# Optimization experiments

Hardware: AMD Instinct MI355X
Metric: run time of the kernel (lower is better)

## Reference

```python
import jax, jax.numpy as jnp
import numpy as np

H = 512      # hidden_size
FF = 4 * H   # expert FFN inner dim
E = 8        # expert_num
K = 2        # top_k
B, S = 4, 4096


def setup_inputs() -> dict:
    key = jax.random.key(0)
    ks = jax.random.split(key, 4)
    s = 0.02
    return {
        "x":  jax.random.normal(ks[0], (B, S, H), dtype=jnp.float32),
        "Wg": jax.random.normal(ks[1], (H, E), dtype=jnp.float32) * s,
        "bg": jnp.zeros((E,), dtype=jnp.float32),
        "W1": jax.random.normal(ks[2], (E, H, FF), dtype=jnp.float32) * s,
        "b1": jnp.zeros((E, FF), dtype=jnp.float32),
        "W2": jax.random.normal(ks[3], (E, FF, H), dtype=jnp.float32) * s,
        "b2": jnp.zeros((E, H), dtype=jnp.float32),
    }


def reference(x, Wg, bg, W1, b1, W2, b2):
    # gate + top-k routing
    logits = x @ Wg + bg                               # [B,S,E]
    w, idx = jax.lax.top_k(logits, K)                  # [B,S,K]
    w = jax.nn.softmax(w, axis=-1)                     # softmax over top-k logits

    # naive dense MoE: every expert runs on every token (matches torch source)
    h = jax.nn.silu(jnp.einsum('bsh,ehf->ebsf', x, W1) + b1[:, None, None, :])  # [E,B,S,FF]
    y = jnp.einsum('ebsf,efh->ebsh', h, W2) + b2[:, None, None, :]              # [E,B,S,H]

    # one-hot mask * top-k weight, combined over slots (same math as torch loop)
    comb = jnp.einsum('bske,bsk->ebs', jax.nn.one_hot(idx, E, dtype=x.dtype), w)  # [E,B,S]
    return jnp.einsum('ebsh,ebs->bsh', y, comb)        # [B,S,H]
```

## Files before the change

kernel.cpp:

```cpp
#include <hip/hip_runtime.h>
#include <hip/hip_bf16.h>
#include <math.h>


#define T_TOK 16384
#define H_DIM 512
#define FF_DIM 2048
#define E_NUM 8
#define NSLOT (T_TOK * 2)
#define NB_ROUTE 128

typedef __attribute__((ext_vector_type(4))) float f32x4;
typedef __attribute__((ext_vector_type(8))) short s16x8;

__device__ __forceinline__ void gload_lds16(const void* g, void* l) {
    __builtin_amdgcn_global_load_lds((const __attribute__((address_space(1))) void*)g,
                                     (__attribute__((address_space(3))) void*)l, 16, 0, 0);
}

__device__ __forceinline__ unsigned short f2bf(float f) {
    union { float f; unsigned int u; } a; a.f = f;
    unsigned int r = a.u + 0x7FFF + ((a.u >> 16) & 1);
    return (unsigned short)(r >> 16);
}


__global__ __launch_bounds__(256) void zero_f32(float* p, int n) {
    int i = (blockIdx.x * 256 + threadIdx.x) * 4;
    if (i < n) { f32x4 z = {0.f, 0.f, 0.f, 0.f}; *(f32x4*)(p + i) = z; }
}

__global__ __launch_bounds__(256) void transpose_bf16(const float* __restrict__ src,
                                                      unsigned short* __restrict__ dst,
                                                      int R, int C) {
    const int e = blockIdx.z;
    const int c0 = blockIdx.x * 32, r0 = blockIdx.y * 32;
    __shared__ float tile[32][33];
    const float* s = src + (size_t)e * R * C;
    unsigned short* d = dst + (size_t)e * R * C;
    const int tid = threadIdx.x;
    for (int idx = tid; idx < 1024; idx += 256) {
        int r = idx >> 5, c = idx & 31;
        tile[r][c] = s[(size_t)(r0 + r) * C + c0 + c];
    }
    __syncthreads();
    for (int idx = tid; idx < 1024; idx += 256) {
        int r = idx >> 5, c = idx & 31;
        d[(size_t)(c0 + r) * R + r0 + c] = f2bf(tile[c][r]);
    }
}

__global__ __launch_bounds__(256) void gather_a(const unsigned short* __restrict__ xb,
                                                const int* __restrict__ slot_token,
                                                unsigned short* __restrict__ Ax) {
    const int gid = blockIdx.x * 256 + threadIdx.x;
    const int s = gid >> 6;
    const int o = (gid & 63) * 8;
    const int t = slot_token[s];
    *(s16x8*)&Ax[(size_t)s * H_DIM + o] = *(const s16x8*)&xb[(size_t)t * H_DIM + o];
}


__global__ __launch_bounds__(256) void gate_topk(const float* __restrict__ x,
                                                 const float* __restrict__ Wg,
                                                 const float* __restrict__ bg,
                                                 int* __restrict__ eidx,
                                                 float* __restrict__ ewt,
                                                 unsigned short* __restrict__ xb) {
    const int t = blockIdx.x * 4 + (threadIdx.x >> 6);
    const int l = threadIdx.x & 63;
    const float* xr = x + (size_t)t * H_DIM;
    unsigned short* xw = xb + (size_t)t * H_DIM;
    double part[E_NUM];
#pragma unroll
    for (int e = 0; e < E_NUM; ++e) part[e] = 0.0;
#pragma unroll
    for (int i = 0; i < 8; ++i) {
        const int h = l + 64 * i;
        const float xv = xr[h];
        xw[h] = f2bf(xv);
        const double xd = (double)xv;
        const float* wr = Wg + (size_t)h * E_NUM;
#pragma unroll
        for (int e = 0; e < E_NUM; ++e) part[e] += xd * (double)wr[e];
    }
    for (int s = 1; s < 64; s <<= 1) {
#pragma unroll
        for (int e = 0; e < E_NUM; ++e) part[e] += __shfl_xor(part[e], s);
    }
    if (l == 0) {
        double lg[E_NUM];
#pragma unroll
        for (int e = 0; e < E_NUM; ++e) lg[e] = part[e] + (double)bg[e];
        int e0 = 0;
        for (int e = 1; e < E_NUM; ++e) if (lg[e] > lg[e0]) e0 = e;
        int e1 = (e0 == 0) ? 1 : 0;
        for (int e = 0; e < E_NUM; ++e) if (e != e0 && lg[e] > lg[e1]) e1 = e;
        double z = exp(lg[e1] - lg[e0]);
        float w0 = (float)(1.0 / (1.0 + z));
        float w1 = (float)(z / (1.0 + z));
        eidx[2 * t] = e0; eidx[2 * t + 1] = e1;
        ewt[2 * t] = w0; ewt[2 * t + 1] = w1;
    }
}


__global__ __launch_bounds__(256) void count_blocks(const int* __restrict__ eidx,
                                                    int* __restrict__ blockcnt) {
    __shared__ int cnt[E_NUM];
    if (threadIdx.x < E_NUM) cnt[threadIdx.x] = 0;
    __syncthreads();
    const int s = blockIdx.x * 256 + threadIdx.x;
    atomicAdd(&cnt[eidx[s]], 1);
    __syncthreads();
    if (threadIdx.x < E_NUM)
        blockcnt[blockIdx.x * E_NUM + threadIdx.x] = cnt[threadIdx.x];
}

__global__ __launch_bounds__(512) void scan_blocks(const int* __restrict__ blockcnt,
                                                   int* __restrict__ bbase,
                                                   int* __restrict__ offsets) {
    __shared__ int tot[E_NUM];
    __shared__ int obase[E_NUM + 1];
    const int e = threadIdx.x >> 6;
    const int l = threadIdx.x & 63;
    const int a = blockcnt[(2 * l) * E_NUM + e];
    const int b = blockcnt[(2 * l + 1) * E_NUM + e];
    const int s = a + b;
    int sc = s;
    for (int d = 1; d < 64; d <<= 1) {
        int o = __shfl_up(sc, d);
        if (l >= d) sc += o;
    }
    const int excl = sc - s;
    if (l == 63) tot[e] = sc;
    __syncthreads();
    if (threadIdx.x == 0) {
        int acc = 0;
        for (int i = 0; i < E_NUM; ++i) { obase[i] = acc; acc += tot[i]; }
        obase[E_NUM] = acc;
        for (int i = 0; i <= E_NUM; ++i) offsets[i] = obase[i];
    }
    __syncthreads();
    const int base = obase[e] + excl;
    bbase[(2 * l) * E_NUM + e] = base;
    bbase[(2 * l + 1) * E_NUM + e] = base + a;
}

__global__ __launch_bounds__(256) void scatter_slots(const int* __restrict__ eidx,
                                                     const float* __restrict__ ewt,
                                                     const int* __restrict__ bbase,
                                                     int* __restrict__ slot_token,
                                                     float* __restrict__ slot_w,
                                                     int* __restrict__ slot_of) {
    __shared__ int cur[E_NUM];
    if (threadIdx.x < E_NUM)
        cur[threadIdx.x] = bbase[blockIdx.x * E_NUM + threadIdx.x];
    __syncthreads();
    const int s = blockIdx.x * 256 + threadIdx.x;
    const int e = eidx[s];
    const int pos = atomicAdd(&cur[e], 1);
    slot_token[pos] = s >> 1;
    slot_w[pos] = ewt[s];
    slot_of[s] = pos;
}


template<int EPI, int GAT, int NT, int KD, int NTOT, int MC, int LDA>
__global__ __launch_bounds__(256, 3) void ggemm(
    const unsigned short* __restrict__ Ag,
    const unsigned short* __restrict__ Bt,
    const float* __restrict__ bias,
    const int* __restrict__ slot_token,
    const float* __restrict__ slot_w,
    const int* __restrict__ offsets,
    unsigned short* __restrict__ Hout,
    float* __restrict__ out) {
    const int e = blockIdx.x;
    const int nt = blockIdx.y % NT;
    const int mc = blockIdx.y / NT;
    const int base = offsets[e];
    const int cnt = offsets[e + 1] - base;
    if (cnt == 0) return;
    const int n0 = nt * 128;

    __shared__ __align__(16) unsigned short Abuf[128 * 64];
    __shared__ __align__(16) unsigned short Bbuf[128 * 64];

    const int tid = threadIdx.x;
    const int w = tid >> 6;
    const int l = tid & 63;
    const int wm = (w & 1) << 6;
    const int wn = (w >> 1) << 6;

    int aoff[4], boff[4];
#pragma unroll
    for (int i = 0; i < 4; ++i) {
        int r = wm + i * 16 + (l & 15);
        aoff[i] = r * 128 + ((((l >> 4) ^ (r & 7))) << 4);
    }
#pragma unroll
    for (int j = 0; j < 4; ++j) {
        int r = wn + j * 16 + (l & 15);
        boff[j] = r * 128 + ((((l >> 4) ^ (r & 7))) << 4);
    }

    const int srow = tid >> 3;
    const int sce = (tid & 7) * 8;
    const unsigned short* Bg = Bt + (size_t)e * NTOT * KD + (size_t)n0 * KD;
    const int nk = KD / 64;

    int bsrc[4];
#pragma unroll
    for (int p = 0; p < 4; ++p) {
        int row = p * 32 + srow;
        bsrc[p] = (row & ~63) | ((row & 15) << 2) | ((row >> 4) & 3);
    }

    for (int m0 = mc * 128; m0 < cnt; m0 += MC * 128) {
        int arow[4];
#pragma unroll
        for (int p = 0; p < 4; ++p) {
            int s = m0 + p * 32 + srow;
            if (s > cnt - 1) s = cnt - 1;
            arow[p] = GAT ? slot_token[base + s] : (base + s);
        }

        f32x4 acc[4][4] = {};
        for (int kt = 0; kt < nk; ++kt) {
            const int k0 = kt * 64;
            __syncthreads();
#pragma unroll
            for (int p = 0; p < 4; ++p) {
                int row = p * 32 + srow;
                int ce = sce ^ ((row & 7) * 8);
                gload_lds16(Ag + (size_t)arow[p] * LDA + k0 + ce, &Abuf[row * 64 + sce]);
                gload_lds16(Bg + (size_t)bsrc[p] * KD + k0 + ce, &Bbuf[row * 64 + sce]);
            }
            __syncthreads();
            const char* Ab = (const char*)&Abuf[0];
            const char* Bb = (const char*)&Bbuf[0];
#pragma unroll
            for (int half = 0; half < 2; ++half) {
                const int kb = half << 6;
                s16x8 af[4], bfv[4];
#pragma unroll
                for (int i = 0; i < 4; ++i) af[i] = *(const s16x8*)(Ab + (aoff[i] ^ kb));
#pragma unroll
                for (int j = 0; j < 4; ++j) bfv[j] = *(const s16x8*)(Bb + (boff[j] ^ kb));
#pragma unroll
                for (int i = 0; i < 4; ++i)
#pragma unroll
                    for (int j = 0; j < 4; ++j)
                        acc[i][j] = __builtin_amdgcn_mfma_f32_16x16x32_bf16(af[i], bfv[j], acc[i][j], 0, 0, 0);
            }
        }

        const int c0 = wn + (l & 15) * 4;
        float b4[4];
#pragma unroll
        for (int j = 0; j < 4; ++j) b4[j] = bias[(size_t)e * NTOT + n0 + c0 + j];

#pragma unroll
        for (int i = 0; i < 4; ++i) {
            const int rb = wm + i * 16 + ((l >> 4) << 2);
#pragma unroll
            for (int r = 0; r < 4; ++r) {
                const int row = m0 + rb + r;
                if (row >= cnt) continue;
                const int slot = base + row;
                if (EPI == 0) {
                    float v0 = acc[i][0][r] + b4[0];
                    float v1 = acc[i][1][r] + b4[1];
                    float v2 = acc[i][2][r] + b4[2];
                    float v3 = acc[i][3][r] + b4[3];
                    v0 = v0 / (1.0f + __expf(-v0));
                    v1 = v1 / (1.0f + __expf(-v1));
                    v2 = v2 / (1.0f + __expf(-v2));
                    v3 = v3 / (1.0f + __expf(-v3));
                    uint2 pk;
                    pk.x = (unsigned int)f2bf(v0) | ((unsigned int)f2bf(v1) << 16);
                    pk.y = (unsigned int)f2bf(v2) | ((unsigned int)f2bf(v3) << 16);
                    *(uint2*)&Hout[(size_t)slot * NTOT + n0 + c0] = pk;
                } else if (EPI == 2) {
                    const float wgt = slot_w[slot];
                    f32x4 v;
#pragma unroll
                    for (int j = 0; j < 4; ++j) v[j] = wgt * (acc[i][j][r] + b4[j]);
                    *(f32x4*)&out[(size_t)slot * NTOT + n0 + c0] = v;
                } else {
                    const int tok = slot_token[slot];
                    const float wgt = slot_w[slot];
                    float* op = out + (size_t)tok * NTOT + n0 + c0;
#pragma unroll
                    for (int j = 0; j < 4; ++j)
                        atomicAdd(op + j, wgt * (acc[i][j][r] + b4[j]));
                }
            }
        }
        __syncthreads();
    }
}

__global__ __launch_bounds__(256) void combine_y(const float* __restrict__ Y,
                                                 const int* __restrict__ slot_of,
                                                 float* __restrict__ out) {
    const int idx = blockIdx.x * 256 + threadIdx.x;
    const int t = idx >> 6;
    const int h = (idx & 63) * 8;
    const int sa = slot_of[2 * t];
    const int sb = slot_of[2 * t + 1];
    const float* pa = Y + (size_t)sa * H_DIM + h;
    const float* pb = Y + (size_t)sb * H_DIM + h;
    f32x4 a0 = *(const f32x4*)pa, a1 = *(const f32x4*)(pa + 4);
    f32x4 b0 = *(const f32x4*)pb, b1 = *(const f32x4*)(pb + 4);
    float* po = out + (size_t)t * H_DIM + h;
    *(f32x4*)po = a0 + b0;
    *(f32x4*)(po + 4) = a1 + b1;
}


extern "C" void kernel_launch(void* const* d_in, const int* in_sizes, int n_in,
                              void* d_out, int out_size, void* d_ws, size_t ws_size,
                              hipStream_t stream) {
    const float* x  = (const float*)d_in[0];
    const float* Wg = (const float*)d_in[1];
    const float* bg = (const float*)d_in[2];
    const float* W1 = (const float*)d_in[3];
    const float* b1 = (const float*)d_in[4];
    const float* W2 = (const float*)d_in[5];
    const float* b2 = (const float*)d_in[6];
    float* out = (float*)d_out;

    char* ws = (char*)d_ws;
    size_t off = 0;
    auto take = [&](size_t b) -> void* {
        void* p = ws + off;
        off = (off + b + 255) & ~(size_t)255;
        return p;
    };
    unsigned short* xb   = (unsigned short*)take((size_t)T_TOK * H_DIM * 2);
    unsigned short* W1t  = (unsigned short*)take((size_t)E_NUM * H_DIM * FF_DIM * 2);
    unsigned short* W2t  = (unsigned short*)take((size_t)E_NUM * H_DIM * FF_DIM * 2);
    int*   eidx       = (int*)take((size_t)T_TOK * 2 * 4);
    float* ewt        = (float*)take((size_t)T_TOK * 2 * 4);
    int*   slot_token = (int*)take((size_t)NSLOT * 4);
    float* slot_w     = (float*)take((size_t)NSLOT * 4);
    int*   slot_of    = (int*)take((size_t)NSLOT * 4);
    int*   blockcnt   = (int*)take((size_t)NB_ROUTE * E_NUM * 4);
    int*   bbase      = (int*)take((size_t)NB_ROUTE * E_NUM * 4);
    int*   offsets    = (int*)take(256);
    unsigned short* Hact = (unsigned short*)take((size_t)NSLOT * FF_DIM * 2);
    float* Yf = (float*)take((size_t)NSLOT * H_DIM * 4);
    const int useY = (ws_size >= off) ? 1 : 0;
    unsigned short* Ax = (unsigned short*)(ws + off);
    const int useAx = (ws_size >= off + (size_t)NSLOT * H_DIM * 2) ? 1 : 0;

    transpose_bf16<<<dim3(FF_DIM / 32, H_DIM / 32, E_NUM), 256, 0, stream>>>(W1, W1t, H_DIM, FF_DIM);
    transpose_bf16<<<dim3(H_DIM / 32, FF_DIM / 32, E_NUM), 256, 0, stream>>>(W2, W2t, FF_DIM, H_DIM);

    gate_topk<<<T_TOK / 4, 256, 0, stream>>>(x, Wg, bg, eidx, ewt, xb);
    count_blocks<<<NB_ROUTE, 256, 0, stream>>>(eidx, blockcnt);
    scan_blocks<<<1, 512, 0, stream>>>(blockcnt, bbase, offsets);
    scatter_slots<<<NB_ROUTE, 256, 0, stream>>>(eidx, ewt, bbase, slot_token, slot_w, slot_of);

    if (useAx) {
        gather_a<<<NSLOT * 64 / 256, 256, 0, stream>>>(xb, slot_token, Ax);
        ggemm<0, 0, 16, 512, 2048, 16, 512><<<dim3(8, 256), 256, 0, stream>>>(
            Ax, W1t, b1, slot_token, slot_w, offsets, Hact, out);
    } else {
        ggemm<0, 1, 16, 512, 2048, 16, 512><<<dim3(8, 256), 256, 0, stream>>>(
            xb, W1t, b1, slot_token, slot_w, offsets, Hact, out);
    }
    if (useY) {
        ggemm<2, 0, 4, 2048, 512, 32, 2048><<<dim3(8, 128), 256, 0, stream>>>(
            Hact, W2t, b2, slot_token, slot_w, offsets, Hact, Yf);
        combine_y<<<T_TOK * 64 / 256, 256, 0, stream>>>(Yf, slot_of, out);
    } else {
        zero_f32<<<(T_TOK * H_DIM / 4 + 255) / 256, 256, 0, stream>>>(out, T_TOK * H_DIM);
        ggemm<1, 0, 4, 2048, 512, 32, 2048><<<dim3(8, 128), 256, 0, stream>>>(
            Hact, W2t, b2, slot_token, slot_w, offsets, Hact, out);
    }
    (void)in_sizes; (void)n_in; (void)out_size;
}
```

Baseline: 318.8 us.

## Enlarge grouped GEMM tiles to 256x256 with double-buffered LDS prefetch

Rewrites the grouped expert GEMM to use 512-thread blocks computing 256x256 tiles, with LDS double buffering. Global-to-LDS loads for the next K tiles are interleaved with MFMA quarters, using explicit vmcnt waits, barriers and setprio. The larger tiles are meant to raise data reuse and hide memory latency behind compute. In exchange, occupancy drops to one block per CU with 128KB of LDS, and the much smaller grid (e.g. 8x32 blocks for the second GEMM) may leave CUs idle given per-expert imbalance.

Result: slower. 421.2 us (+32.1%).

```diff
diff --git a/kernel.cpp b/kernel.cpp
--- a/kernel.cpp
+++ b/kernel.cpp
@@ -166,8 +166,8 @@
 }
 
 
-template<int EPI, int GAT, int NT, int KD, int NTOT, int MC, int LDA>
-__global__ __launch_bounds__(256, 3) void ggemm(
+template<int EPI, int GAT, int NT, int KD, int NTOT, int MCB, int LDA>
+__global__ __launch_bounds__(512, 1) void ggemm(
     const unsigned short* __restrict__ Ag,
     const unsigned short* __restrict__ Bt,
     const float* __restrict__ bias,
@@ -182,20 +182,20 @@
     const int base = offsets[e];
     const int cnt = offsets[e + 1] - base;
     if (cnt == 0) return;
-    const int n0 = nt * 128;
-
-    __shared__ __align__(16) unsigned short Abuf[128 * 64];
-    __shared__ __align__(16) unsigned short Bbuf[128 * 64];
+    const int n0 = nt * 256;
+
+    __shared__ __align__(16) unsigned short Abuf[2][256 * 64];
+    __shared__ __align__(16) unsigned short Bbuf[2][256 * 64];
 
     const int tid = threadIdx.x;
     const int w = tid >> 6;
     const int l = tid & 63;
-    const int wm = (w & 1) << 6;
-    const int wn = (w >> 1) << 6;
-
-    int aoff[4], boff[4];
-#pragma unroll
-    for (int i = 0; i < 4; ++i) {
+    const int wm = (w >> 2) << 7;
+    const int wn = (w & 3) << 6;
+
+    int aoff[8], boff[4];
+#pragma unroll
+    for (int i = 0; i < 8; ++i) {
         int r = wm + i * 16 + (l & 15);
         aoff[i] = r * 128 + ((((l >> 4) ^ (r & 7))) << 4);
     }
@@ -207,54 +207,93 @@
 
     const int srow = tid >> 3;
     const int sce = (tid & 7) * 8;
+    int srow4[4], sceX[4];
+#pragma unroll
+    for (int p = 0; p < 4; ++p) {
+        srow4[p] = p * 64 + srow;
+        sceX[p] = sce ^ ((srow4[p] & 7) * 8);
+    }
     const unsigned short* Bg = Bt + (size_t)e * NTOT * KD + (size_t)n0 * KD;
     const int nk = KD / 64;
 
     int bsrc[4];
 #pragma unroll
     for (int p = 0; p < 4; ++p) {
-        int row = p * 32 + srow;
+        int row = srow4[p];
         bsrc[p] = (row & ~63) | ((row & 15) << 2) | ((row >> 4) & 3);
     }
 
-    for (int m0 = mc * 128; m0 < cnt; m0 += MC * 128) {
+    for (int m0 = mc * 256; m0 < cnt; m0 += MCB * 256) {
         int arow[4];
 #pragma unroll
         for (int p = 0; p < 4; ++p) {
-            int s = m0 + p * 32 + srow;
+            int s = m0 + srow4[p];
             if (s > cnt - 1) s = cnt - 1;
             arow[p] = GAT ? slot_token[base + s] : (base + s);
         }
 
-        f32x4 acc[4][4] = {};
+#define STAGE_A(tile, p) gload_lds16(Ag + (size_t)arow[p] * LDA + (tile) * 64 + sceX[p], \
+                                     &Abuf[(tile) & 1][srow4[p] * 64 + sce])
+#define STAGE_B(tile, p) gload_lds16(Bg + (size_t)bsrc[p] * KD + (tile) * 64 + sceX[p], \
+                                     &Bbuf[(tile) & 1][srow4[p] * 64 + sce])
+
+#pragma unroll
+        for (int p = 0; p < 4; ++p) { STAGE_A(0, p); STAGE_B(0, p); }
+#pragma unroll
+        for (int p = 0; p < 4; ++p) STAGE_B(1, p);
+        STAGE_A(1, 0); STAGE_A(1, 2);
+        asm volatile("s_waitcnt vmcnt(6)" ::: "memory");
+        __builtin_amdgcn_s_barrier();
+
+        f32x4 acc[8][4] = {};
         for (int kt = 0; kt < nk; ++kt) {
-            const int k0 = kt * 64;
-            __syncthreads();
-#pragma unroll
-            for (int p = 0; p < 4; ++p) {
-                int row = p * 32 + srow;
-                int ce = sce ^ ((row & 7) * 8);
-                gload_lds16(Ag + (size_t)arow[p] * LDA + k0 + ce, &Abuf[row * 64 + sce]);
-                gload_lds16(Bg + (size_t)bsrc[p] * KD + k0 + ce, &Bbuf[row * 64 + sce]);
-            }
-            __syncthreads();
-            const char* Ab = (const char*)&Abuf[0];
-            const char* Bb = (const char*)&Bbuf[0];
-#pragma unroll
-            for (int half = 0; half < 2; ++half) {
-                const int kb = half << 6;
-                s16x8 af[4], bfv[4];
-#pragma unroll
-                for (int i = 0; i < 4; ++i) af[i] = *(const s16x8*)(Ab + (aoff[i] ^ kb));
-#pragma unroll
-                for (int j = 0; j < 4; ++j) bfv[j] = *(const s16x8*)(Bb + (boff[j] ^ kb));
-#pragma unroll
-                for (int i = 0; i < 4; ++i)
-#pragma unroll
-                    for (int j = 0; j < 4; ++j)
-                        acc[i][j] = __builtin_amdgcn_mfma_f32_16x16x32_bf16(af[i], bfv[j], acc[i][j], 0, 0, 0);
+            const char* Ab = (const char*)&Abuf[kt & 1][0];
+            const char* Bb = (const char*)&Bbuf[kt & 1][0];
+            s16x8 bfv[2][4];
+#pragma unroll
+            for (int q = 0; q < 4; ++q) {
+                if (q == 0) {
+#pragma unroll
+                    for (int h = 0; h < 2; ++h)
+#pragma unroll
+                        for (int j = 0; j < 4; ++j)
+                            bfv[h][j] = *(const s16x8*)(Bb + (boff[j] ^ (h << 6)));
+                }
+                s16x8 af[2][2];
+#pragma unroll
+                for (int ii = 0; ii < 2; ++ii)
+#pragma unroll
+                    for (int h = 0; h < 2; ++h)
+                        af[ii][h] = *(const s16x8*)(Ab + (aoff[2 * q + ii] ^ (h << 6)));
+                if (q == 0) {
+                    if (kt + 1 < nk) { STAGE_A(kt + 1, 1); STAGE_A(kt + 1, 3); }
+                } else if (q == 1) {
+                    if (kt + 2 < nk) { STAGE_B(kt + 2, 0); STAGE_B(kt + 2, 1); }
+                } else if (q == 2) {
+                    if (kt + 2 < nk) { STAGE_B(kt + 2, 2); STAGE_B(kt + 2, 3); }
+                } else {
+                    if (kt + 2 < nk) { STAGE_A(kt + 2, 0); STAGE_A(kt + 2, 2); }
+                }
+                __builtin_amdgcn_s_barrier();
+                __builtin_amdgcn_s_setprio(1);
+#pragma unroll
+                for (int h = 0; h < 2; ++h)
+#pragma unroll
+                    for (int ii = 0; ii < 2; ++ii)
+#pragma unroll
+                        for (int j = 0; j < 4; ++j)
+                            acc[2 * q + ii][j] = __builtin_amdgcn_mfma_f32_16x16x32_bf16(
+                                af[ii][h], bfv[h][j], acc[2 * q + ii][j], 0, 0, 0);
+                __builtin_amdgcn_s_setprio(0);
+                if (q == 3) {
+                    if (kt + 2 < nk) asm volatile("s_waitcnt vmcnt(6)" ::: "memory");
+                    else             asm volatile("s_waitcnt vmcnt(0)" ::: "memory");
+                }
+                __builtin_amdgcn_s_barrier();
             }
         }
+#undef STAGE_A
+#undef STAGE_B
 
         const int c0 = wn + (l & 15) * 4;
         float b4[4];
@@ -262,7 +301,7 @@
         for (int j = 0; j < 4; ++j) b4[j] = bias[(size_t)e * NTOT + n0 + c0 + j];
 
 #pragma unroll
-        for (int i = 0; i < 4; ++i) {
+        for (int i = 0; i < 8; ++i) {
             const int rb = wm + i * 16 + ((l >> 4) << 2);
 #pragma unroll
             for (int r = 0; r < 4; ++r) {
@@ -366,19 +405,19 @@
 
     if (useAx) {
         gather_a<<<NSLOT * 64 / 256, 256, 0, stream>>>(xb, slot_token, Ax);
-        ggemm<0, 0, 16, 512, 2048, 16, 512><<<dim3(8, 256), 256, 0, stream>>>(
+        ggemm<0, 0, 8, 512, 2048, 16, 512><<<dim3(8, 128), 512, 0, stream>>>(
             Ax, W1t, b1, slot_token, slot_w, offsets, Hact, out);
     } else {
-        ggemm<0, 1, 16, 512, 2048, 16, 512><<<dim3(8, 256), 256, 0, stream>>>(
+        ggemm<0, 1, 8, 512, 2048, 16, 512><<<dim3(8, 128), 512, 0, stream>>>(
             xb, W1t, b1, slot_token, slot_w, offsets, Hact, out);
     }
     if (useY) {
-        ggemm<2, 0, 4, 2048, 512, 32, 2048><<<dim3(8, 128), 256, 0, stream>>>(
+        ggemm<2, 0, 2, 2048, 512, 16, 2048><<<dim3(8, 32), 512, 0, stream>>>(
             Hact, W2t, b2, slot_token, slot_w, offsets, Hact, Yf);
         combine_y<<<T_TOK * 64 / 256, 256, 0, stream>>>(Yf, slot_of, out);
     } else {
         zero_f32<<<(T_TOK * H_DIM / 4 + 255) / 256, 256, 0, stream>>>(out, T_TOK * H_DIM);
-        ggemm<1, 0, 4, 2048, 512, 32, 2048><<<dim3(8, 128), 256, 0, stream>>>(
+        ggemm<1, 0, 2, 2048, 512, 16, 2048><<<dim3(8, 32), 512, 0, stream>>>(
             Hact, W2t, b2, slot_token, slot_w, offsets, Hact, out);
     }
     (void)in_sizes; (void)n_in; (void)out_size;
```

## Software-pipeline grouped GEMM with triple-buffered A and double-buffered B in LDS

Applied to the files above, without the earlier changes.

Replaces the single-buffered load-then-compute loop with a prefetch pipeline: A tiles are loaded two k-steps ahead into a 3-slot LDS ring and B tiles one step ahead into a 2-slot ring. Fine-grained vmcnt waits plus one barrier per iteration replace the two __syncthreads. The goal is to overlap global-to-LDS latency with MFMA work. The cost is 2.5x the LDS per block, and the launch bound's minimum-occupancy hint of 3 blocks is dropped, which can lower occupancy.

New measurement: 379.9 us. +19.2%, slower.

```diff
diff --git a/kernel.cpp b/kernel.cpp
--- a/kernel.cpp
+++ b/kernel.cpp
@@ -167,7 +167,7 @@
 
 
 template<int EPI, int GAT, int NT, int KD, int NTOT, int MC, int LDA>
-__global__ __launch_bounds__(256, 3) void ggemm(
+__global__ __launch_bounds__(256) void ggemm(
     const unsigned short* __restrict__ Ag,
     const unsigned short* __restrict__ Bt,
     const float* __restrict__ bias,
@@ -184,8 +184,8 @@
     if (cnt == 0) return;
     const int n0 = nt * 128;
 
-    __shared__ __align__(16) unsigned short Abuf[128 * 64];
-    __shared__ __align__(16) unsigned short Bbuf[128 * 64];
+    __shared__ __align__(16) unsigned short Abuf[3][128 * 64];
+    __shared__ __align__(16) unsigned short Bbuf[2][128 * 64];
 
     const int tid = threadIdx.x;
     const int w = tid >> 6;
@@ -226,20 +226,35 @@
             arow[p] = GAT ? slot_token[base + s] : (base + s);
         }
 
+#define STAGE_A(kt, buf) do { \
+    for (int p = 0; p < 4; ++p) { \
+        int row = p * 32 + srow; \
+        int ce = sce ^ ((row & 7) * 8); \
+        gload_lds16(Ag + (size_t)arow[p] * LDA + (kt) * 64 + ce, &Abuf[buf][row * 64 + sce]); \
+    } } while (0)
+#define STAGE_B(kt, buf) do { \
+    for (int p = 0; p < 4; ++p) { \
+        int row = p * 32 + srow; \
+        int ce = sce ^ ((row & 7) * 8); \
+        gload_lds16(Bg + (size_t)bsrc[p] * KD + (kt) * 64 + ce, &Bbuf[buf][row * 64 + sce]); \
+    } } while (0)
+
+        STAGE_A(0, 0);
+        STAGE_B(0, 0);
+        if (nk > 1) STAGE_A(1, 1);
+        asm volatile("s_waitcnt vmcnt(4)" ::: "memory");
+        __builtin_amdgcn_s_barrier();
+        asm volatile("" ::: "memory");
+
         f32x4 acc[4][4] = {};
+        int ia = 0;
         for (int kt = 0; kt < nk; ++kt) {
-            const int k0 = kt * 64;
-            __syncthreads();
-#pragma unroll
-            for (int p = 0; p < 4; ++p) {
-                int row = p * 32 + srow;
-                int ce = sce ^ ((row & 7) * 8);
-                gload_lds16(Ag + (size_t)arow[p] * LDA + k0 + ce, &Abuf[row * 64 + sce]);
-                gload_lds16(Bg + (size_t)bsrc[p] * KD + k0 + ce, &Bbuf[row * 64 + sce]);
-            }
-            __syncthreads();
-            const char* Ab = (const char*)&Abuf[0];
-            const char* Bb = (const char*)&Bbuf[0];
+            const int ia2 = (ia + 2 >= 3) ? ia - 1 : ia + 2;
+            if (kt + 1 < nk) STAGE_B(kt + 1, (kt + 1) & 1);
+            if (kt + 2 < nk) STAGE_A(kt + 2, ia2);
+
+            const char* Ab = (const char*)&Abuf[ia][0];
+            const char* Bb = (const char*)&Bbuf[kt & 1][0];
 #pragma unroll
             for (int half = 0; half < 2; ++half) {
                 const int kb = half << 6;
@@ -254,7 +269,17 @@
                     for (int j = 0; j < 4; ++j)
                         acc[i][j] = __builtin_amdgcn_mfma_f32_16x16x32_bf16(af[i], bfv[j], acc[i][j], 0, 0, 0);
             }
+            if (kt + 2 < nk) {
+                asm volatile("s_waitcnt vmcnt(4)" ::: "memory");
+            } else {
+                asm volatile("s_waitcnt vmcnt(0)" ::: "memory");
+            }
+            __builtin_amdgcn_s_barrier();
+            asm volatile("" ::: "memory");
+            ia = (ia == 2) ? 0 : ia + 1;
         }
+#undef STAGE_A
+#undef STAGE_B
 
         const int c0 = wn + (l & 15) * 4;
         float b4[4];
```
